# Kernel tuning notes

Measured on AMD Instinct MI355X. Metric: run time of the kernel, lower is better.

Reference implementation:

```python
import math
import jax, jax.numpy as jnp
import numpy as np

# cfg constants
IMG_W, IMG_H, CENTER_H = 800.0, 320.0, 160.0
NUM_OFFSETS = 72
ANGLE_THRES, RHO_THRES = 0.5, 0.5
CONF_THRES_O2O = 0.4
H_DIM, I_DIM, IOU_DIM = 64, 128, 1


def _lin(x, W, b):
    return x @ W + b


def setup_inputs() -> dict:
    B, N = 4, 512
    key = jax.random.key(0)
    ks = jax.random.split(key, 24)
    s = 0.05
    inp = {
        "batch_features": jax.random.normal(ks[0], (B, N, H_DIM), jnp.float32),
        "cls_pred": jax.random.uniform(ks[1], (B, N), jnp.float32),
        "anchor_id": jnp.tile(jnp.arange(N, dtype=jnp.int32), (B, 1)),
        "anchor_embeddings": 0.1 + 0.3 * jax.random.uniform(ks[2], (B, N, 2), jnp.float32),
        # cls_block
        "W_cls": s * jax.random.normal(ks[3], (H_DIM, H_DIM)), "b_cls": jnp.zeros((H_DIM,)),
        # LaneGNN
        "W_pos": s * jax.random.normal(ks[4], (2, I_DIM)), "b_pos": jnp.zeros((I_DIM,)),
        "W_in": s * jax.random.normal(ks[5], (H_DIM, I_DIM)), "b_in": jnp.zeros((I_DIM,)),
        "W_out": s * jax.random.normal(ks[6], (H_DIM, I_DIM)), "b_out": jnp.zeros((I_DIM,)),
        "W_e1": s * jax.random.normal(ks[7], (I_DIM, I_DIM)), "b_e1": jnp.zeros((I_DIM,)),
        "W_e2": s * jax.random.normal(ks[8], (I_DIM, IOU_DIM)), "b_e2": jnp.zeros((IOU_DIM,)),
        "W_n1": s * jax.random.normal(ks[9], (IOU_DIM, H_DIM)), "b_n1": jnp.zeros((H_DIM,)),
        "W_n2": s * jax.random.normal(ks[10], (H_DIM, H_DIM)), "b_n2": jnp.zeros((H_DIM,)),
        # cls_layer
        "W_head": s * jax.random.normal(ks[11], (H_DIM, 1)), "b_head": jnp.zeros((1,)),
    }
    return inp


def _get_nbr_mask(emb):
    angle = emb[..., 0] * math.pi
    rho = emb[..., 1] * IMG_W  # computed but unused due to original code's bug
    a = jnp.abs(angle[..., :, None] - angle[..., None, :])
    a = jnp.triu(a, k=1)
    a = a + jnp.swapaxes(a, -1, -2)
    # NOTE: faithful to original bug - rho matrix is rebuilt from the angle matrix
    r = jnp.triu(a, k=1)
    r = r + jnp.swapaxes(r, -1, -2)
    return (a < ANGLE_THRES) & (r < RHO_THRES)


def _get_sample_point(emb):
    B, N = emb.shape[0], emb.shape[1]
    e = emb.reshape(-1, 2)
    angle = e[:, 0] * math.pi
    rho = e[:, 1] * IMG_W
    lin = jnp.linspace(0.0, 1.0 - 1e-5, NUM_OFFSETS, dtype=jnp.float32)
    sample_car_y = (CENTER_H - lin * IMG_H)[:2]  # buffer keeps first 2
    x = -jnp.tan(angle)[:, None] * sample_car_y[None, :] + (rho / jnp.cos(angle))[:, None]
    return x.reshape(B, N, 2) / IMG_W


def reference(batch_features, cls_pred, anchor_id, anchor_embeddings,
              W_cls, b_cls, W_pos, b_pos, W_in, b_in, W_out, b_out,
              W_e1, b_e1, W_e2, b_e2, W_n1, b_n1, W_n2, b_n2, W_head, b_head):
    # suppression matrix (no-grad region in torch)
    nbr_masks = _get_nbr_mask(anchor_embeddings)
    cls_mat = cls_pred[..., :, None] - cls_pred[..., None, :]
    id_mat = (anchor_id[..., :, None] - anchor_id[..., None, :]).astype(jnp.float32)
    supress = ((cls_mat > 0) | ((cls_mat == 0) & (id_mat > 0))).astype(jnp.float32)
    supress = jnp.where(nbr_masks, supress, 0.0)
    pos_emb = _get_sample_point(anchor_embeddings)              # [B,N,2]
    pos_emb_mat = pos_emb[:, :, None, :] - pos_emb[:, None, :, :]  # [B,N,N,2]

    # cls_block
    feats = jax.nn.relu(_lin(batch_features, W_cls, b_cls))     # [B,N,H]

    # LaneGNN
    f_in = _lin(feats, W_in, b_in)    # [B,N,I]
    f_out = _lin(feats, W_out, b_out)  # [B,N,I]
    edge_emb = _lin(pos_emb_mat, W_pos, b_pos)  # [B,N,N,I]
    edge = f_in[:, :, None, :] - f_out[:, None, :, :] + edge_emb
    edge = _lin(jax.nn.gelu(_lin(edge, W_e1, b_e1), approximate=False), W_e2, b_e2)  # [B,N,N,iou]
    edge = edge * supress[..., None]
    node_max = jnp.max(edge, axis=1)  # [B,N,iou]
    node = jax.nn.relu(_lin(node_max, W_n1, b_n1))
    node = jax.nn.relu(_lin(node, W_n2, b_n2))

    logits = _lin(node, W_head, b_head)[..., 0]  # [B,N]
    logits = jnp.where(cls_pred < CONF_THRES_O2O, -1e6, logits)
    return jax.nn.sigmoid(logits)
```

## Files before the change

kernel.cpp:

```cpp
#include <hip/hip_runtime.h>
#include <math.h>

#define B  4
#define N  512
#define BN (B * N)
#define H  64
#define I  128

#define PI_F   3.14159265358979323846f
#define Y0_F   160.0f
#define Y1_F   155.4930028f
#define INV_W  (1.0f / 800.0f)

__device__ __forceinline__ float gelu_fast(float x) {
    float x2 = x * x;
    float t1 = __builtin_fmaf(x2, -2.0f * 0.0356774081f, -2.0f * 0.7978845608f);
    float e  = __expf(x * t1);
    return x * __builtin_amdgcn_rcpf(1.0f + e);
}

#define NPB 4

__global__ __launch_bounds__(256) void prep_kernel(
    const float* __restrict__ bf, const float* __restrict__ emb,
    const float* __restrict__ W_cls, const float* __restrict__ b_cls,
    const float* __restrict__ W_pos, const float* __restrict__ b_pos,
    const float* __restrict__ W_in,  const float* __restrict__ b_in,
    const float* __restrict__ W_out, const float* __restrict__ b_out,
    const float* __restrict__ W_e1,  const float* __restrict__ b_e1,
    float* __restrict__ Uo, float* __restrict__ Vo)
{
    __shared__ float sbf[NPB][64];
    __shared__ float sft[NPB][64];
    __shared__ float su[NPB][128];
    __shared__ float sv[NPB][128];
    __shared__ float sp[NPB][2];

    const int tid = threadIdx.x;
    const int node0 = blockIdx.x * NPB;

    {
        int nd = tid >> 6, d = tid & 63;
        sbf[nd][d] = bf[(node0 + nd) * 64 + d];
    }
    if (tid < NPB) {
        int g = node0 + tid;
        float ang = emb[g * 2] * PI_F;
        float t = tanf(ang);
        float rc = (emb[g * 2 + 1] * 800.0f) / cosf(ang);
        sp[tid][0] = (-t * Y0_F + rc) * INV_W;
        sp[tid][1] = (-t * Y1_F + rc) * INV_W;
    }
    __syncthreads();

    {
        int nd = tid >> 6, h = tid & 63;
        float a0 = 0.f, a1 = 0.f, a2 = 0.f, a3 = 0.f;
        #pragma unroll 4
        for (int d = 0; d < 64; d += 4) {
            a0 += sbf[nd][d + 0] * W_cls[(d + 0) * 64 + h];
            a1 += sbf[nd][d + 1] * W_cls[(d + 1) * 64 + h];
            a2 += sbf[nd][d + 2] * W_cls[(d + 2) * 64 + h];
            a3 += sbf[nd][d + 3] * W_cls[(d + 3) * 64 + h];
        }
        sft[nd][h] = fmaxf(b_cls[h] + ((a0 + a1) + (a2 + a3)), 0.0f);
    }
    __syncthreads();

    {
        int k = tid & 127, np = tid >> 7;
        int n0 = np * 2, n1 = n0 + 1;
        float wp0 = W_pos[k], wp1 = W_pos[128 + k];
        float pe0 = sp[n0][0] * wp0 + sp[n0][1] * wp1;
        float pe1 = sp[n1][0] * wp0 + sp[n1][1] * wp1;
        float bi = b_in[k] + b_pos[k], bo = b_out[k];
        float au0 = 0.f, av0 = 0.f, au1 = 0.f, av1 = 0.f;
        #pragma unroll 8
        for (int h = 0; h < 64; ++h) {
            float wi = W_in[h * 128 + k];
            float wo = W_out[h * 128 + k];
            float f0 = sft[n0][h], f1 = sft[n1][h];
            au0 += f0 * wi;  av0 += f0 * wo;
            au1 += f1 * wi;  av1 += f1 * wo;
        }
        su[n0][k] = au0 + bi + pe0;  sv[n0][k] = av0 + bo + pe0;
        su[n1][k] = au1 + bi + pe1;  sv[n1][k] = av1 + bo + pe1;
    }
    __syncthreads();

    {
        int k = tid & 127, np = tid >> 7;
        int n0 = np * 2, n1 = n0 + 1;
        float aU0 = 0.f, aV0 = 0.f, aU1 = 0.f, aV1 = 0.f;
        #pragma unroll 8
        for (int m = 0; m < 128; ++m) {
            float w = W_e1[m * 128 + k];
            aU0 += su[n0][m] * w;  aV0 += sv[n0][m] * w;
            aU1 += su[n1][m] * w;  aV1 += sv[n1][m] * w;
        }
        float be = b_e1[k];
        Uo[(node0 + n0) * 128 + k] = aU0 + be;
        Vo[(node0 + n0) * 128 + k] = aV0;
        Uo[(node0 + n1) * 128 + k] = aU1 + be;
        Vo[(node0 + n1) * 128 + k] = aV1;
    }
}

__global__ __launch_bounds__(256) void edge_kernel(
    const float* __restrict__ U, const float* __restrict__ V,
    const float* __restrict__ cls, const int* __restrict__ aid,
    const float* __restrict__ emb,
    const float* __restrict__ W_e2, const float* __restrict__ b_e2,
    const float* __restrict__ W_n1, const float* __restrict__ b_n1,
    const float* __restrict__ W_n2, const float* __restrict__ b_n2,
    const float* __restrict__ W_hd, const float* __restrict__ b_hd,
    float* __restrict__ out)
{
    const int col  = blockIdx.x;
    const int tid  = threadIdx.x;
    const int wave = tid >> 6;
    const int lane = tid & 63;

    __shared__ float Vs[128];
    __shared__ float w2s[128];
    __shared__ unsigned short lseg[4][128];
    __shared__ unsigned short list[512];
    __shared__ int wcnt[4];
    __shared__ float red[4];
    __shared__ float n1s[64];

    const float cls_j = cls[col];
    if (cls_j < 0.4f) {
        if (tid == 0) out[col] = 0.0f;
        return;
    }

    if (tid < 128) {
        Vs[tid]  = V[col * 128 + tid];
        w2s[tid] = W_e2[tid];
    }

    const int   rowbase = (col >> 9) << 9;
    const float ang_j   = emb[col * 2] * PI_F;
    const int   id_j    = aid[col];
    const float be2     = b_e2[0];

    int c = 0;
    #pragma unroll
    for (int rr = 0; rr < 2; ++rr) {
        int i  = wave * 128 + rr * 64 + lane;
        int gi = rowbase + i;
        float ci = cls[gi];
        bool m = (ci > cls_j) || (ci == cls_j && aid[gi] > id_j);
        if (m) m = fabsf(emb[gi * 2] * PI_F - ang_j) < 0.5f;
        unsigned long long bal = __ballot(m);
        int pre = __popcll(bal & ((1ull << lane) - 1ull));
        if (m) lseg[wave][c + pre] = (unsigned short)i;
        c += __popcll(bal);
    }
    if (lane == 0) wcnt[wave] = c;
    __syncthreads();

    const int c0 = wcnt[0], c1 = wcnt[1], c2 = wcnt[2], c3 = wcnt[3];
    const int o1 = c0, o2 = c0 + c1, o3 = o2 + c2;
    const int total = o3 + c3;
    for (int r = tid; r < c0; r += 256) list[r]      = lseg[0][r];
    for (int r = tid; r < c1; r += 256) list[o1 + r] = lseg[1][r];
    for (int r = tid; r < c2; r += 256) list[o2 + r] = lseg[2][r];
    for (int r = tid; r < c3; r += 256) list[o3 + r] = lseg[3][r];
    __syncthreads();

    float wm = 0.0f;
    const float4* V4 = (const float4*)Vs;
    const float4* g4 = (const float4*)w2s;
    for (int r = tid; r < total; r += 256) {
        int gi = rowbase + (int)list[r];
        const float4* Up = (const float4*)(U + gi * 128);
        float s0 = 0.f, s1 = 0.f, s2 = 0.f, s3 = 0.f;
        #pragma unroll 8
        for (int k4 = 0; k4 < 32; ++k4) {
            float4 u4 = Up[k4];
            float4 v4 = V4[k4];
            float4 w4 = g4[k4];
            s0 += gelu_fast(u4.x - v4.x) * w4.x;
            s1 += gelu_fast(u4.y - v4.y) * w4.y;
            s2 += gelu_fast(u4.z - v4.z) * w4.z;
            s3 += gelu_fast(u4.w - v4.w) * w4.w;
        }
        wm = fmaxf(wm, ((s0 + s1) + (s2 + s3)) + be2);
    }

    #pragma unroll
    for (int off = 32; off > 0; off >>= 1)
        wm = fmaxf(wm, __shfl_down(wm, off));
    if (lane == 0) red[wave] = wm;
    __syncthreads();

    if (wave == 0) {
        const float nm = fmaxf(fmaxf(red[0], red[1]), fmaxf(red[2], red[3]));
        n1s[lane] = fmaxf(nm * W_n1[lane] + b_n1[lane], 0.0f);
        float a = b_n2[lane];
        #pragma unroll 8
        for (int m2 = 0; m2 < 64; ++m2) a += n1s[m2] * W_n2[m2 * 64 + lane];
        a = fmaxf(a, 0.0f);
        float p = a * W_hd[lane];
        #pragma unroll
        for (int off = 32; off > 0; off >>= 1) p += __shfl_down(p, off);
        if (lane == 0) {
            float logit = p + b_hd[0];
            out[col] = 1.0f / (1.0f + expf(-logit));
        }
    }
}

extern "C" void kernel_launch(void* const* d_in, const int* in_sizes, int n_in,
                              void* d_out, int out_size, void* d_ws, size_t ws_size,
                              hipStream_t stream) {
    const float* bf    = (const float*)d_in[0];
    const float* cls   = (const float*)d_in[1];
    const int*   aid   = (const int*)  d_in[2];
    const float* emb   = (const float*)d_in[3];
    const float* W_cls = (const float*)d_in[4];
    const float* b_cls = (const float*)d_in[5];
    const float* W_pos = (const float*)d_in[6];
    const float* b_pos = (const float*)d_in[7];
    const float* W_in  = (const float*)d_in[8];
    const float* b_in  = (const float*)d_in[9];
    const float* W_out = (const float*)d_in[10];
    const float* b_out = (const float*)d_in[11];
    const float* W_e1  = (const float*)d_in[12];
    const float* b_e1  = (const float*)d_in[13];
    const float* W_e2  = (const float*)d_in[14];
    const float* b_e2  = (const float*)d_in[15];
    const float* W_n1  = (const float*)d_in[16];
    const float* b_n1  = (const float*)d_in[17];
    const float* W_n2  = (const float*)d_in[18];
    const float* b_n2  = (const float*)d_in[19];
    const float* W_hd  = (const float*)d_in[20];
    const float* b_hd  = (const float*)d_in[21];

    float* Uw = (float*)d_ws;
    float* Vw = Uw + BN * I;
    float* out = (float*)d_out;

    prep_kernel<<<BN / NPB, 256, 0, stream>>>(
        bf, emb, W_cls, b_cls, W_pos, b_pos, W_in, b_in, W_out, b_out,
        W_e1, b_e1, Uw, Vw);
    edge_kernel<<<BN, 256, 0, stream>>>(
        Uw, Vw, cls, aid, emb, W_e2, b_e2, W_n1, b_n1, W_n2, b_n2,
        W_hd, b_hd, out);
}
```

Baseline: 133.2 us.

## Split edge dot products across half-waves with coalesced row loads

```diff
diff --git a/kernel.cpp b/kernel.cpp
--- a/kernel.cpp
+++ b/kernel.cpp
@@ -140,7 +140,7 @@
         w2s[tid] = W_e2[tid];
     }
 
-    const int   rowbase = (col >> 9) << 9;
+    const int   rowbase = col & ~(N - 1);
     const float ang_j   = emb[col * 2] * PI_F;
     const int   id_j    = aid[col];
     const float be2     = b_e2[0];
@@ -171,23 +171,30 @@
     __syncthreads();
 
     float wm = 0.0f;
-    const float4* V4 = (const float4*)Vs;
-    const float4* g4 = (const float4*)w2s;
-    for (int r = tid; r < total; r += 256) {
-        int gi = rowbase + (int)list[r];
-        const float4* Up = (const float4*)(U + gi * 128);
-        float s0 = 0.f, s1 = 0.f, s2 = 0.f, s3 = 0.f;
-        #pragma unroll 8
-        for (int k4 = 0; k4 < 32; ++k4) {
-            float4 u4 = Up[k4];
-            float4 v4 = V4[k4];
-            float4 w4 = g4[k4];
-            s0 += gelu_fast(u4.x - v4.x) * w4.x;
-            s1 += gelu_fast(u4.y - v4.y) * w4.y;
-            s2 += gelu_fast(u4.z - v4.z) * w4.z;
-            s3 += gelu_fast(u4.w - v4.w) * w4.w;
-        }
-        wm = fmaxf(wm, ((s0 + s1) + (s2 + s3)) + be2);
+    const int sub = lane >> 5;
+    const int l5  = lane & 31;
+    const int npairs = (total + 1) >> 1;
+    for (int p = wave; p < npairs; p += 4) {
+        int ia = 2 * p;
+        int ib = (ia + 1 < total) ? (ia + 1) : ia;
+        int row = (int)list[sub ? ib : ia];
+        const float4* Up = (const float4*)(U + (size_t)(rowbase + row) * 128) + l5;
+        float4 u4 = *Up;
+        int k = l5 * 4;
+        float s;
+        {
+            float t0 = gelu_fast(u4.x - Vs[k + 0]) * w2s[k + 0];
+            float t1 = gelu_fast(u4.y - Vs[k + 1]) * w2s[k + 1];
+            float t2 = gelu_fast(u4.z - Vs[k + 2]) * w2s[k + 2];
+            float t3 = gelu_fast(u4.w - Vs[k + 3]) * w2s[k + 3];
+            s = (t0 + t1) + (t2 + t3);
+        }
+        s += __shfl_xor(s, 1);
+        s += __shfl_xor(s, 2);
+        s += __shfl_xor(s, 4);
+        s += __shfl_xor(s, 8);
+        s += __shfl_xor(s, 16);
+        wm = fmaxf(wm, s + be2);
     }
 
     #pragma unroll
```

New measurement: 131.6 us. No clear change (-1.2%).
